# Optimization experiments

Hardware: AMD Instinct MI355X
Metric: run time of the kernel (lower is better)

Reference implementation:

```python
import jax, jax.numpy as jnp
import numpy as np

D = 256; NH = 8; NL = 4; NP = 4; DFF = 2048; HD = D // NH
SHAPES = [(64, 64), (32, 32), (16, 16), (8, 8)]
B = 2; LEN = sum(h * w for h, w in SHAPES)


def setup_inputs() -> dict:
    key = jax.random.key(0)
    ks = jax.random.split(key, 12)
    def w(k, shape, s=0.02):
        return jax.random.normal(k, shape, jnp.float32) * s
    starts = np.cumsum([0] + [h * w for h, w in SHAPES[:-1]])
    return {
        "src": jax.random.normal(ks[0], (B, LEN, D), jnp.float32),
        "pos": jax.random.normal(ks[1], (B, LEN, D), jnp.float32) * 0.1,
        "spatial_shapes": jnp.array(SHAPES, dtype=jnp.int32),
        "level_start_index": jnp.array(starts, dtype=jnp.int32),
        "w_value": w(ks[2], (D, D)), "b_value": jnp.zeros((D,), jnp.float32),
        "w_off": w(ks[3], (D, NH * NL * NP * 2)), "b_off": w(ks[4], (NH * NL * NP * 2,), 0.1),
        "w_attn": w(ks[5], (D, NH * NL * NP)), "b_attn": jnp.zeros((NH * NL * NP,), jnp.float32),
        "w_out": w(ks[6], (D, D)), "b_out": jnp.zeros((D,), jnp.float32),
        "w1": w(ks[7], (D, DFF)), "b1": jnp.zeros((DFF,), jnp.float32),
        "w2": w(ks[8], (DFF, D)), "b2": jnp.zeros((D,), jnp.float32),
        "g1": jnp.ones((D,), jnp.float32), "be1": jnp.zeros((D,), jnp.float32),
        "g2": jnp.ones((D,), jnp.float32), "be2": jnp.zeros((D,), jnp.float32),
    }


def _layer_norm(x, g, b):
    mu = jnp.mean(x, -1, keepdims=True)
    v = jnp.var(x, -1, keepdims=True)
    return (x - mu) * jax.lax.rsqrt(v + 1e-5) * g + b


def _reference_points(shapes):
    # torch.linspace(0.5, H-0.5, H)/H == (arange(H)+0.5)/H
    refs = []
    for H, W in shapes:
        ry = (jnp.arange(H, dtype=jnp.float32) + 0.5) / H
        rx = (jnp.arange(W, dtype=jnp.float32) + 0.5) / W
        yy, xx = jnp.meshgrid(ry, rx, indexing='ij')
        refs.append(jnp.stack([xx.ravel(), yy.ravel()], -1))
    return jnp.concatenate(refs, 0)  # (Len, 2) as (x, y)


def _ms_deform_sample(value, loc, shapes):
    # value: (B, Len, NH, HD); loc: (B, Lq, NH, NL, NP, 2) normalized [0,1]
    # Replicates torch grid_sample(bilinear, padding='zeros', align_corners=False).
    Bn, Lq = loc.shape[0], loc.shape[1]
    P = loc.shape[4]
    start = 0
    outs = []
    for lvl, (H, W) in enumerate(shapes):
        v = value[:, start:start + H * W].transpose(0, 2, 1, 3)  # (B, NH, HW, HD)
        start += H * W
        l = loc[:, :, :, lvl]                      # (B, Lq, NH, P, 2)
        x = l[..., 0] * W - 0.5
        y = l[..., 1] * H - 0.5
        x0 = jnp.floor(x); y0 = jnp.floor(y)
        dx = x - x0; dy = y - y0
        x0i = x0.astype(jnp.int32); y0i = y0.astype(jnp.int32)
        acc = None
        for xi, yi, wgt in ((x0i, y0i, (1 - dx) * (1 - dy)),
                            (x0i + 1, y0i, dx * (1 - dy)),
                            (x0i, y0i + 1, (1 - dx) * dy),
                            (x0i + 1, y0i + 1, dx * dy)):
            valid = ((xi >= 0) & (xi < W) & (yi >= 0) & (yi < H)).astype(value.dtype)
            idx = jnp.clip(yi, 0, H - 1) * W + jnp.clip(xi, 0, W - 1)  # (B, Lq, NH, P)
            idx = idx.transpose(0, 2, 1, 3).reshape(Bn, NH, Lq * P)
            g = jnp.take_along_axis(v, idx[..., None], axis=2).reshape(Bn, NH, Lq, P, HD)
            w = (wgt * valid).transpose(0, 2, 1, 3)[..., None]  # (B, NH, Lq, P, 1)
            acc = g * w if acc is None else acc + g * w
        outs.append(acc)  # (B, NH, Lq, P, HD)
    return jnp.stack(outs, 3)  # (B, NH, Lq, NL, NP, HD)


def _forward(src, pos, w_value, b_value, w_off, b_off, w_attn, b_attn,
             w_out, b_out, w1, b1, w2, b2, g1, be1, g2, be2, shapes):
    Bn, Lq, _ = src.shape
    q = src + pos  # with_pos_embed
    value = (src @ w_value + b_value).reshape(Bn, Lq, NH, HD)
    off = (q @ w_off + b_off).reshape(Bn, Lq, NH, NL, NP, 2)
    attn = jax.nn.softmax((q @ w_attn + b_attn).reshape(Bn, Lq, NH, NL * NP), -1)
    attn = attn.reshape(Bn, Lq, NH, NL, NP)
    ref = _reference_points(shapes)  # (Len, 2)
    normalizer = jnp.array([[w_, h_] for h_, w_ in shapes], jnp.float32)  # (NL, 2) = (W, H)
    loc = ref[None, :, None, None, None, :] + off / normalizer[None, None, None, :, None, :]
    sampled = _ms_deform_sample(value, loc, shapes)  # (B, NH, Lq, NL, NP, HD)
    out = jnp.einsum('bqhlp,bhqlpd->bqhd', attn, sampled).reshape(Bn, Lq, D)
    out = out @ w_out + b_out
    x = _layer_norm(src + out, g1, be1)           # residual + norm1
    ff = jax.nn.relu(x @ w1 + b1) @ w2 + b2       # FFN (dropout=0)
    return _layer_norm(x + ff, g2, be2)           # residual + norm2


def reference(src, pos, spatial_shapes, level_start_index, w_value, b_value,
              w_off, b_off, w_attn, b_attn, w_out, b_out, w1, b1, w2, b2,
              g1, be1, g2, be2):
    shapes = [tuple(int(v) for v in s) for s in np.asarray(spatial_shapes)]
    return _forward(src, pos, w_value, b_value, w_off, b_off, w_attn, b_attn,
                    w_out, b_out, w1, b1, w2, b2, g1, be1, g2, be2, shapes)
```

## Files before the change

### kernel.cpp

```cpp
#include <hip/hip_runtime.h>
#include <math.h>

#define D 256
#define NH 8
#define NL 4
#define NP 4
#define DFF 2048
#define HD 32
#define BB 2
#define LEN 5440
#define MROWS (BB * LEN)

typedef __attribute__((ext_vector_type(8))) short short8;
typedef __attribute__((ext_vector_type(4))) float f32x4;
typedef unsigned int uint32;

__device__ __forceinline__ unsigned short f2bf(float f) {
    uint32 u = __float_as_uint(f);
    u += 0x7FFF + ((u >> 16) & 1);
    return (unsigned short)(u >> 16);
}
__device__ __forceinline__ float bf2f(unsigned short h) {
    return __uint_as_float(((uint32)h) << 16);
}
__device__ __forceinline__ uint32 pack2(float a, float b) {
    return (uint32)f2bf(a) | ((uint32)f2bf(b) << 16);
}

__device__ __forceinline__ void swz85(int b, int ncols, int& row, int& col) {
    const int gsz = ncols << 3;
    const int full = 10 * gsz;
    if (b < full) {
        const int g = b / gsz, idx = b - g * gsz;
        row = (g << 3) + (idx & 7);
        col = idx >> 3;
    } else {
        const int idx = b - full;
        row = 80 + idx % 5;
        col = idx / 5;
    }
}

__global__ void prep(const float* __restrict__ w_value, const float* __restrict__ w_off,
                     const float* __restrict__ w_attn, const float* __restrict__ w_out,
                     const float* __restrict__ w1, const float* __restrict__ w2,
                     const float* __restrict__ b_value, const float* __restrict__ b_off,
                     const float* __restrict__ b_attn,
                     unsigned short* __restrict__ wqvT, unsigned short* __restrict__ woT,
                     unsigned short* __restrict__ w1T, unsigned short* __restrict__ w2T,
                     float* __restrict__ bqv) {
    const int blk = blockIdx.x;
    if (blk >= 1248) {
        for (int i = threadIdx.x; i < 640; i += 256)
            bqv[i] = (i < 256) ? b_value[i] : (i < 512 ? b_off[i - 256] : b_attn[i - 512]);
        return;
    }
    const float* W; unsigned short* WT; int K, N, tid;
    if (blk < 64)       { W = w_value; WT = wqvT;             K = 256;  N = 256;  tid = blk; }
    else if (blk < 128) { W = w_off;   WT = wqvT + 256 * 256; K = 256;  N = 256;  tid = blk - 64; }
    else if (blk < 160) { W = w_attn;  WT = wqvT + 512 * 256; K = 256;  N = 128;  tid = blk - 128; }
    else if (blk < 224) { W = w_out;   WT = woT;              K = 256;  N = 256;  tid = blk - 160; }
    else if (blk < 736) { W = w1;      WT = w1T;              K = 256;  N = 2048; tid = blk - 224; }
    else                { W = w2;      WT = w2T;              K = 2048; N = 256;  tid = blk - 736; }
    const int ntx = N >> 5;
    const int nb = (tid % ntx) * 32, kb = (tid / ntx) * 32;

    __shared__ float tile[32][33];
    const int tx = threadIdx.x & 31, ty = threadIdx.x >> 5;
#pragma unroll
    for (int i = 0; i < 32; i += 8)
        tile[ty + i][tx] = W[(size_t)(kb + ty + i) * N + nb + tx];
    __syncthreads();
#pragma unroll
    for (int i = 0; i < 32; i += 8)
        WT[(size_t)(nb + ty + i) * K + kb + tx] = f2bf(tile[tx][ty + i]);
}

__global__ __launch_bounds__(256) void ffn1_gemm(
        const unsigned short* __restrict__ A,
        const unsigned short* __restrict__ BT, const float* __restrict__ bias,
        unsigned short* __restrict__ Cv, int N, int K, int lda, int ldb) {
    __shared__ unsigned short Ash[128][40];
    __shared__ unsigned short Bsh[128][40];

    int rowt, colt;
    swz85(blockIdx.x, N >> 7, rowt, colt);
    const int row0 = rowt * 128, col0 = colt * 128;

    const int t = threadIdx.x;
    const int wave = t >> 6, lane = t & 63;
    const int wr = wave >> 1, wc = wave & 1;
    const int lrow = lane & 15, quad = lane >> 4;
    const int srow = t >> 1;
    const int cb = (t & 1) * 16;

    const unsigned short* ap = A + (size_t)(row0 + srow) * lda + cb;
    const unsigned short* bp = BT + (size_t)(col0 + srow) * ldb + cb;

    f32x4 acc[4][4];
#pragma unroll
    for (int i = 0; i < 4; i++)
#pragma unroll
        for (int j = 0; j < 4; j++) acc[i][j] = (f32x4){0.f, 0.f, 0.f, 0.f};

    uint4 ra0 = *(const uint4*)(ap + 0), ra1 = *(const uint4*)(ap + 8);
    uint4 rb0 = *(const uint4*)(bp + 0), rb1 = *(const uint4*)(bp + 8);

    for (int kb = 0; kb < K; kb += 32) {
        __syncthreads();
        *(uint4*)&Ash[srow][cb + 0] = ra0;
        *(uint4*)&Ash[srow][cb + 8] = ra1;
        *(uint4*)&Bsh[srow][cb + 0] = rb0;
        *(uint4*)&Bsh[srow][cb + 8] = rb1;
        __syncthreads();
        if (kb + 32 < K) {
            ra0 = *(const uint4*)(ap + kb + 32 + 0);
            ra1 = *(const uint4*)(ap + kb + 32 + 8);
            rb0 = *(const uint4*)(bp + kb + 32 + 0);
            rb1 = *(const uint4*)(bp + kb + 32 + 8);
        }

        short8 af[4], bfr[4];
#pragma unroll
        for (int mt = 0; mt < 4; mt++)
            af[mt] = *(const short8*)&Ash[wr * 64 + mt * 16 + lrow][quad * 8];
#pragma unroll
        for (int nt = 0; nt < 4; nt++)
            bfr[nt] = *(const short8*)&Bsh[wc * 64 + nt * 16 + lrow][quad * 8];
#pragma unroll
        for (int mt = 0; mt < 4; mt++)
#pragma unroll
            for (int nt = 0; nt < 4; nt++)
                acc[mt][nt] = __builtin_amdgcn_mfma_f32_16x16x32_bf16(
                    af[mt], bfr[nt], acc[mt][nt], 0, 0, 0);
    }

#pragma unroll
    for (int nt = 0; nt < 4; nt++) {
        const int col = col0 + wc * 64 + nt * 16 + lrow;
        const float bv = bias[col];
#pragma unroll
        for (int mt = 0; mt < 4; mt++) {
            f32x4 a = acc[mt][nt];
#pragma unroll
            for (int r = 0; r < 4; r++) {
                const int row = row0 + wr * 64 + mt * 16 + quad * 4 + r;
                Cv[(size_t)row * N + col] = f2bf(fmaxf(a[r] + bv, 0.f));
            }
        }
    }
}

template <int NZ>
__global__ __launch_bounds__(256) void splitk_gemm(
        const unsigned short* __restrict__ A, const unsigned short* __restrict__ BT,
        float* __restrict__ part, int KC, int lda, int ldb) {
    __shared__ unsigned short Ash[128][40];
    __shared__ unsigned short Bsh[128][40];

    int rowt, cc;
    swz85(blockIdx.x, 2 * NZ, rowt, cc);
    const int row0 = rowt * 128;
    const int col0 = (cc & 1) * 128;
    const int z = cc >> 1;
    const int koff = z * KC;
    float* __restrict__ C = part + (size_t)z * MROWS * 256;

    const int t = threadIdx.x;
    const int wave = t >> 6, lane = t & 63;
    const int wr = wave >> 1, wc = wave & 1;
    const int lrow = lane & 15, quad = lane >> 4;
    const int srow = t >> 1;
    const int cb = (t & 1) * 16;

    const unsigned short* ap = A + (size_t)(row0 + srow) * lda + koff + cb;
    const unsigned short* bp = BT + (size_t)(col0 + srow) * ldb + koff + cb;

    f32x4 acc[4][4];
#pragma unroll
    for (int i = 0; i < 4; i++)
#pragma unroll
        for (int j = 0; j < 4; j++) acc[i][j] = (f32x4){0.f, 0.f, 0.f, 0.f};

    uint4 ra0 = *(const uint4*)(ap + 0), ra1 = *(const uint4*)(ap + 8);
    uint4 rb0 = *(const uint4*)(bp + 0), rb1 = *(const uint4*)(bp + 8);

    for (int kb = 0; kb < KC; kb += 32) {
        __syncthreads();
        *(uint4*)&Ash[srow][cb + 0] = ra0;
        *(uint4*)&Ash[srow][cb + 8] = ra1;
        *(uint4*)&Bsh[srow][cb + 0] = rb0;
        *(uint4*)&Bsh[srow][cb + 8] = rb1;
        __syncthreads();
        if (kb + 32 < KC) {
            ra0 = *(const uint4*)(ap + kb + 32 + 0);
            ra1 = *(const uint4*)(ap + kb + 32 + 8);
            rb0 = *(const uint4*)(bp + kb + 32 + 0);
            rb1 = *(const uint4*)(bp + kb + 32 + 8);
        }

        short8 af[4], bfr[4];
#pragma unroll
        for (int mt = 0; mt < 4; mt++)
            af[mt] = *(const short8*)&Ash[wr * 64 + mt * 16 + lrow][quad * 8];
#pragma unroll
        for (int nt = 0; nt < 4; nt++)
            bfr[nt] = *(const short8*)&Bsh[wc * 64 + nt * 16 + lrow][quad * 8];
#pragma unroll
        for (int mt = 0; mt < 4; mt++)
#pragma unroll
            for (int nt = 0; nt < 4; nt++)
                acc[mt][nt] = __builtin_amdgcn_mfma_f32_16x16x32_bf16(
                    af[mt], bfr[nt], acc[mt][nt], 0, 0, 0);
    }

#pragma unroll
    for (int nt = 0; nt < 4; nt++) {
        const int col = col0 + wc * 64 + nt * 16 + lrow;
#pragma unroll
        for (int mt = 0; mt < 4; mt++) {
            f32x4 a = acc[mt][nt];
#pragma unroll
            for (int r = 0; r < 4; r++) {
                const int row = row0 + wr * 64 + mt * 16 + quad * 4 + r;
                C[(size_t)row * 256 + col] = a[r];
            }
        }
    }
}

__global__ __launch_bounds__(256) void qv_gemm(
        const float* __restrict__ src, const float* __restrict__ pos,
        const unsigned short* __restrict__ BT, const float* __restrict__ bias,
        unsigned short* __restrict__ val, float* __restrict__ qout) {
    __shared__ unsigned short Ash[128][40];
    __shared__ unsigned short Bsh[128][40];

    int rowt, colt;
    swz85(blockIdx.x, 5, rowt, colt);
    const int row0 = rowt * 128, col0 = colt * 128;
    const bool addp = (col0 >= 256);

    const int t = threadIdx.x;
    const int wave = t >> 6, lane = t & 63;
    const int wr = wave >> 1, wc = wave & 1;
    const int lrow = lane & 15, quad = lane >> 4;
    const int srow = t >> 1;
    const int cb = (t & 1) * 16;

    const float* ap = src + (size_t)(row0 + srow) * 256 + cb;
    const float* pp = pos + (size_t)(row0 + srow) * 256 + cb;
    const unsigned short* bp = BT + (size_t)(col0 + srow) * 256 + cb;

    f32x4 acc[4][4];
#pragma unroll
    for (int i = 0; i < 4; i++)
#pragma unroll
        for (int j = 0; j < 4; j++) acc[i][j] = (f32x4){0.f, 0.f, 0.f, 0.f};

    float4 fa[4]; float4 fp[4]; uint4 rb0, rb1;
#pragma unroll
    for (int j = 0; j < 4; j++) fa[j] = *(const float4*)(ap + 4 * j);
    if (addp) {
#pragma unroll
        for (int j = 0; j < 4; j++) fp[j] = *(const float4*)(pp + 4 * j);
    }
    rb0 = *(const uint4*)(bp + 0);
    rb1 = *(const uint4*)(bp + 8);

    for (int kb = 0; kb < 256; kb += 32) {
        __syncthreads();
        {
            float4 f0 = fa[0], f1 = fa[1], f2 = fa[2], f3 = fa[3];
            if (addp) {
                f0.x += fp[0].x; f0.y += fp[0].y; f0.z += fp[0].z; f0.w += fp[0].w;
                f1.x += fp[1].x; f1.y += fp[1].y; f1.z += fp[1].z; f1.w += fp[1].w;
                f2.x += fp[2].x; f2.y += fp[2].y; f2.z += fp[2].z; f2.w += fp[2].w;
                f3.x += fp[3].x; f3.y += fp[3].y; f3.z += fp[3].z; f3.w += fp[3].w;
            }
            uint4 u0 = make_uint4(pack2(f0.x, f0.y), pack2(f0.z, f0.w),
                                  pack2(f1.x, f1.y), pack2(f1.z, f1.w));
            uint4 u1 = make_uint4(pack2(f2.x, f2.y), pack2(f2.z, f2.w),
                                  pack2(f3.x, f3.y), pack2(f3.z, f3.w));
            *(uint4*)&Ash[srow][cb + 0] = u0;
            *(uint4*)&Ash[srow][cb + 8] = u1;
            *(uint4*)&Bsh[srow][cb + 0] = rb0;
            *(uint4*)&Bsh[srow][cb + 8] = rb1;
        }
        __syncthreads();
        if (kb + 32 < 256) {
#pragma unroll
            for (int j = 0; j < 4; j++) fa[j] = *(const float4*)(ap + kb + 32 + 4 * j);
            if (addp) {
#pragma unroll
                for (int j = 0; j < 4; j++) fp[j] = *(const float4*)(pp + kb + 32 + 4 * j);
            }
            rb0 = *(const uint4*)(bp + kb + 32 + 0);
            rb1 = *(const uint4*)(bp + kb + 32 + 8);
        }

        short8 af[4], bfr[4];
#pragma unroll
        for (int mt = 0; mt < 4; mt++)
            af[mt] = *(const short8*)&Ash[wr * 64 + mt * 16 + lrow][quad * 8];
#pragma unroll
        for (int nt = 0; nt < 4; nt++)
            bfr[nt] = *(const short8*)&Bsh[wc * 64 + nt * 16 + lrow][quad * 8];
#pragma unroll
        for (int mt = 0; mt < 4; mt++)
#pragma unroll
            for (int nt = 0; nt < 4; nt++)
                acc[mt][nt] = __builtin_amdgcn_mfma_f32_16x16x32_bf16(
                    af[mt], bfr[nt], acc[mt][nt], 0, 0, 0);
    }

#pragma unroll
    for (int nt = 0; nt < 4; nt++) {
        const int col = col0 + wc * 64 + nt * 16 + lrow;
        const float bv = bias[col];
#pragma unroll
        for (int mt = 0; mt < 4; mt++) {
            f32x4 a = acc[mt][nt];
#pragma unroll
            for (int r = 0; r < 4; r++) {
                const int row = row0 + wr * 64 + mt * 16 + quad * 4 + r;
                float v = a[r] + bv;
                if (col < 256)
                    val[(size_t)row * 256 + col] = f2bf(v);
                else
                    qout[(size_t)row * 384 + (col - 256)] = v;
            }
        }
    }
}

__global__ void sampler(const unsigned short* __restrict__ val, const float* __restrict__ qout,
                        unsigned short* __restrict__ out) {
    __shared__ __align__(16) int   sIdx[2][128][4];
    __shared__ __align__(16) float sW[2][128][4];
    const int t = threadIdx.x;
    const int sub = t >> 7;
    const int tt = t & 127;
    const int bq = blockIdx.x * 2 + sub;
    const int b = bq / LEN, q = bq % LEN;

    {
        const int h = tt >> 4, p = tt & 15;
        const int l = p >> 2;

        float refx, refy;
        if (q < 4096) {
            int rq = q >> 6, cq = q & 63;
            refx = (cq + 0.5f) * (1.0f / 64.0f);
            refy = (rq + 0.5f) * (1.0f / 64.0f);
        } else if (q < 5120) {
            int qq = q - 4096;
            int rq = qq >> 5, cq = qq & 31;
            refx = (cq + 0.5f) * (1.0f / 32.0f);
            refy = (rq + 0.5f) * (1.0f / 32.0f);
        } else if (q < 5376) {
            int qq = q - 5120;
            int rq = qq >> 4, cq = qq & 15;
            refx = (cq + 0.5f) * (1.0f / 16.0f);
            refy = (rq + 0.5f) * (1.0f / 16.0f);
        } else {
            int qq = q - 5376;
            int rq = qq >> 3, cq = qq & 7;
            refx = (cq + 0.5f) * (1.0f / 8.0f);
            refy = (rq + 0.5f) * (1.0f / 8.0f);
        }

        float lv = qout[(size_t)bq * 384 + 256 + tt];
        float mx = lv;
#pragma unroll
        for (int o = 1; o < 16; o <<= 1) mx = fmaxf(mx, __shfl_xor(mx, o, 16));
        float e = expf(lv - mx);
        float s = e;
#pragma unroll
        for (int o = 1; o < 16; o <<= 1) s += __shfl_xor(s, o, 16);
        const float aw = e / s;

        const float ox = qout[(size_t)bq * 384 + h * 32 + p * 2 + 0];
        const float oy = qout[(size_t)bq * 384 + h * 32 + p * 2 + 1];

        const int LST[4] = {0, 4096, 5120, 5376};
        const int WW = 64 >> l;
        const float rw = 1.0f / (float)WW;

        float x = (refx + ox * rw) * (float)WW - 0.5f;
        float y = (refy + oy * rw) * (float)WW - 0.5f;
        float x0f = floorf(x), y0f = floorf(y);
        float dx = x - x0f, dy = y - y0f;
        int x0 = (int)x0f, y0 = (int)y0f;

        const int base = (b * LEN + LST[l]) * 256 + h * 32;
        int xs[2] = {x0, x0 + 1}, ys[2] = {y0, y0 + 1};
        float wx[2] = {1.f - dx, dx}, wy[2] = {1.f - dy, dy};
        int ic[4]; float wc4[4];
#pragma unroll
        for (int cy = 0; cy < 2; cy++)
#pragma unroll
            for (int cx = 0; cx < 2; cx++) {
                int xi = xs[cx], yi = ys[cy];
                bool vld = (xi >= 0) && (xi < WW) && (yi >= 0) && (yi < WW);
                int xc = min(max(xi, 0), WW - 1);
                int yc = min(max(yi, 0), WW - 1);
                ic[cy * 2 + cx] = base + (yc * WW + xc) * 256;
                wc4[cy * 2 + cx] = vld ? wx[cx] * wy[cy] * aw : 0.f;
            }
        *(int4*)&sIdx[sub][tt][0] = make_int4(ic[0], ic[1], ic[2], ic[3]);
        *(float4*)&sW[sub][tt][0] = make_float4(wc4[0], wc4[1], wc4[2], wc4[3]);
    }
    __syncthreads();

    const int h = tt >> 4, dp = tt & 15;
    const unsigned short* vald = val + 2 * dp;
    float acc0 = 0.f, acc1 = 0.f;
#pragma unroll 4
    for (int p = 0; p < 16; p++) {
        const int r = h * 16 + p;
        int4 iv = *(const int4*)&sIdx[sub][r][0];
        float4 wv = *(const float4*)&sW[sub][r][0];
        uint32 u0 = *(const uint32*)(vald + iv.x);
        uint32 u1 = *(const uint32*)(vald + iv.y);
        uint32 u2 = *(const uint32*)(vald + iv.z);
        uint32 u3 = *(const uint32*)(vald + iv.w);
        acc0 += bf2f((unsigned short)u0) * wv.x + bf2f((unsigned short)u1) * wv.y +
                bf2f((unsigned short)u2) * wv.z + bf2f((unsigned short)u3) * wv.w;
        acc1 += bf2f((unsigned short)(u0 >> 16)) * wv.x + bf2f((unsigned short)(u1 >> 16)) * wv.y +
                bf2f((unsigned short)(u2 >> 16)) * wv.z + bf2f((unsigned short)(u3 >> 16)) * wv.w;
    }
    *(uint32*)&out[(size_t)bq * D + h * HD + 2 * dp] = pack2(acc0, acc1);
}

template <int NPART>
__global__ void add_lnN(const float* __restrict__ part, const float* __restrict__ bias,
                        const float* __restrict__ rsd,
                        const float* __restrict__ g, const float* __restrict__ be,
                        float* __restrict__ out, unsigned short* __restrict__ out16) {
    __shared__ float r1[4], r2[4];
    const int row = blockIdx.x, t = threadIdx.x;
    const size_t i = (size_t)row * D + t;
    float v = bias[t] + rsd[i];
#pragma unroll
    for (int z = 0; z < NPART; z++) v += part[(size_t)z * MROWS * 256 + i];
    float s1 = v, s2 = v * v;
#pragma unroll
    for (int o = 32; o > 0; o >>= 1) {
        s1 += __shfl_down(s1, o, 64);
        s2 += __shfl_down(s2, o, 64);
    }
    if ((t & 63) == 0) { r1[t >> 6] = s1; r2[t >> 6] = s2; }
    __syncthreads();
    float su = r1[0] + r1[1] + r1[2] + r1[3];
    float sq = r2[0] + r2[1] + r2[2] + r2[3];
    float mean = su * (1.0f / D);
    float var = fmaxf(sq * (1.0f / D) - mean * mean, 0.f);
    const float o = (v - mean) * rsqrtf(var + 1e-5f) * g[t] + be[t];
    out[i] = o;
    if (out16) out16[i] = f2bf(o);
}

extern "C" void kernel_launch(void* const* d_in, const int* in_sizes, int n_in,
                              void* d_out, int out_size, void* d_ws, size_t ws_size,
                              hipStream_t stream) {
    const float* src     = (const float*)d_in[0];
    const float* pos     = (const float*)d_in[1];
    const float* w_value = (const float*)d_in[4];
    const float* b_value = (const float*)d_in[5];
    const float* w_off   = (const float*)d_in[6];
    const float* b_off   = (const float*)d_in[7];
    const float* w_attn  = (const float*)d_in[8];
    const float* b_attn  = (const float*)d_in[9];
    const float* w_out   = (const float*)d_in[10];
    const float* b_out   = (const float*)d_in[11];
    const float* w1      = (const float*)d_in[12];
    const float* b1      = (const float*)d_in[13];
    const float* w2      = (const float*)d_in[14];
    const float* b2      = (const float*)d_in[15];
    const float* g1      = (const float*)d_in[16];
    const float* be1     = (const float*)d_in[17];
    const float* g2      = (const float*)d_in[18];
    const float* be2     = (const float*)d_in[19];
    float* out = (float*)d_out;

    size_t off = 0;
    auto alloc = [&](size_t bytes) -> char* {
        char* p = (char*)d_ws + off;
        off += (bytes + 255) & ~(size_t)255;
        return p;
    };
    unsigned short* wqvT = (unsigned short*)alloc((size_t)640 * 256 * 2);
    unsigned short* woT  = (unsigned short*)alloc(256 * 256 * 2);
    unsigned short* w1T  = (unsigned short*)alloc((size_t)2048 * 256 * 2);
    unsigned short* w2T  = (unsigned short*)alloc((size_t)256 * 2048 * 2);
    float* bqv           = (float*)alloc(640 * 4);

    float* qout          = (float*)alloc((size_t)MROWS * 384 * 4);
    unsigned short* val  = (unsigned short*)alloc((size_t)MROWS * 256 * 2);
    unsigned short* attn = (unsigned short*)alloc((size_t)MROWS * 256 * 2);
    unsigned short* hb   = (unsigned short*)alloc((size_t)MROWS * 2048 * 2);
    float* xbuf          = (float*)alloc((size_t)MROWS * 256 * 4);
    unsigned short* xb16 = (unsigned short*)alloc((size_t)MROWS * 256 * 2);
    float* part          = (float*)alloc((size_t)4 * MROWS * 256 * 4);

    prep<<<1249, 256, 0, stream>>>(w_value, w_off, w_attn, w_out, w1, w2,
                                   b_value, b_off, b_attn, wqvT, woT, w1T, w2T, bqv);

    qv_gemm<<<425, 256, 0, stream>>>(src, pos, wqvT, bqv, val, qout);
    sampler<<<MROWS / 2, 256, 0, stream>>>(val, qout, attn);
    splitk_gemm<2><<<340, 256, 0, stream>>>(attn, woT, part, 128, 256, 256);
    add_lnN<2><<<MROWS, 256, 0, stream>>>(part, b_out, src, g1, be1, xbuf, xb16);

    ffn1_gemm<<<1360, 256, 0, stream>>>(xb16, w1T, b1, hb, 2048, 256, 256, 256);
    splitk_gemm<4><<<680, 256, 0, stream>>>(hb, w2T, part, 512, 2048, 2048);
    add_lnN<4><<<MROWS, 256, 0, stream>>>(part, b2, xbuf, g2, be2, out, nullptr);
}
```

Measured before the change: 218.6 us.

## Fuse output GEMMs with bias, residual and LayerNorm in full-row tiles

Replaces the split-K GEMMs plus separate add+LayerNorm kernels with one kernel per stage. Each block computes 32 full rows of 256 columns and does bias, residual, mean/variance reduction and normalization in the epilogue. This removes the fp32 partial-sum buffers and their round trips through memory, and drops two launches. In exchange there is no split-K parallelism: only 340 blocks run, each looping over the full K (2048 for FFN2), and the tiles are small, so MFMA efficiency and occupancy may suffer.

```diff
diff --git a/kernel.cpp b/kernel.cpp
--- a/kernel.cpp
+++ b/kernel.cpp
@@ -151,82 +151,129 @@
     }
 }
 
-template <int NZ>
-__global__ __launch_bounds__(256) void splitk_gemm(
+template <bool WRITE16>
+__global__ __launch_bounds__(256) void gemm_ln(
         const unsigned short* __restrict__ A, const unsigned short* __restrict__ BT,
-        float* __restrict__ part, int KC, int lda, int ldb) {
-    __shared__ unsigned short Ash[128][40];
-    __shared__ unsigned short Bsh[128][40];
-
-    int rowt, cc;
-    swz85(blockIdx.x, 2 * NZ, rowt, cc);
-    const int row0 = rowt * 128;
-    const int col0 = (cc & 1) * 128;
-    const int z = cc >> 1;
-    const int koff = z * KC;
-    float* __restrict__ C = part + (size_t)z * MROWS * 256;
-
+        const float* __restrict__ bias, const float* __restrict__ rsd,
+        const float* __restrict__ g, const float* __restrict__ be,
+        float* __restrict__ out, unsigned short* __restrict__ out16, int K) {
+    __shared__ __align__(16) unsigned short Ash[32][40];
+    __shared__ __align__(16) unsigned short Bsh[256][40];
+    __shared__ float red1[4][32], red2[4][32];
+
+    const int row0 = blockIdx.x * 32;
     const int t = threadIdx.x;
     const int wave = t >> 6, lane = t & 63;
-    const int wr = wave >> 1, wc = wave & 1;
     const int lrow = lane & 15, quad = lane >> 4;
-    const int srow = t >> 1;
-    const int cb = (t & 1) * 16;
-
-    const unsigned short* ap = A + (size_t)(row0 + srow) * lda + koff + cb;
-    const unsigned short* bp = BT + (size_t)(col0 + srow) * ldb + koff + cb;
-
-    f32x4 acc[4][4];
-#pragma unroll
-    for (int i = 0; i < 4; i++)
+
+    const int ar = t >> 3, ac = (t & 7) * 4;
+    const unsigned short* ap = A + (size_t)(row0 + ar) * K + ac;
+    const int br = t >> 1, cb = (t & 1) * 16;
+    const unsigned short* bp0 = BT + (size_t)br * K + cb;
+    const unsigned short* bp1 = BT + (size_t)(128 + br) * K + cb;
+
+    f32x4 acc[2][4];
+#pragma unroll
+    for (int i = 0; i < 2; i++)
 #pragma unroll
         for (int j = 0; j < 4; j++) acc[i][j] = (f32x4){0.f, 0.f, 0.f, 0.f};
 
-    uint4 ra0 = *(const uint4*)(ap + 0), ra1 = *(const uint4*)(ap + 8);
-    uint4 rb0 = *(const uint4*)(bp + 0), rb1 = *(const uint4*)(bp + 8);
-
-    for (int kb = 0; kb < KC; kb += 32) {
+    uint2 ra = *(const uint2*)ap;
+    uint4 rb00 = *(const uint4*)(bp0 + 0), rb01 = *(const uint4*)(bp0 + 8);
+    uint4 rb10 = *(const uint4*)(bp1 + 0), rb11 = *(const uint4*)(bp1 + 8);
+
+    for (int kb = 0; kb < K; kb += 32) {
         __syncthreads();
-        *(uint4*)&Ash[srow][cb + 0] = ra0;
-        *(uint4*)&Ash[srow][cb + 8] = ra1;
-        *(uint4*)&Bsh[srow][cb + 0] = rb0;
-        *(uint4*)&Bsh[srow][cb + 8] = rb1;
+        *(uint2*)&Ash[ar][ac] = ra;
+        *(uint4*)&Bsh[br][cb + 0] = rb00;
+        *(uint4*)&Bsh[br][cb + 8] = rb01;
+        *(uint4*)&Bsh[128 + br][cb + 0] = rb10;
+        *(uint4*)&Bsh[128 + br][cb + 8] = rb11;
         __syncthreads();
-        if (kb + 32 < KC) {
-            ra0 = *(const uint4*)(ap + kb + 32 + 0);
-            ra1 = *(const uint4*)(ap + kb + 32 + 8);
-            rb0 = *(const uint4*)(bp + kb + 32 + 0);
-            rb1 = *(const uint4*)(bp + kb + 32 + 8);
-        }
-
-        short8 af[4], bfr[4];
-#pragma unroll
-        for (int mt = 0; mt < 4; mt++)
-            af[mt] = *(const short8*)&Ash[wr * 64 + mt * 16 + lrow][quad * 8];
+        if (kb + 32 < K) {
+            ra   = *(const uint2*)(ap + kb + 32);
+            rb00 = *(const uint4*)(bp0 + kb + 32 + 0);
+            rb01 = *(const uint4*)(bp0 + kb + 32 + 8);
+            rb10 = *(const uint4*)(bp1 + kb + 32 + 0);
+            rb11 = *(const uint4*)(bp1 + kb + 32 + 8);
+        }
+
+        short8 af[2], bfr[4];
+#pragma unroll
+        for (int mt = 0; mt < 2; mt++)
+            af[mt] = *(const short8*)&Ash[mt * 16 + lrow][quad * 8];
 #pragma unroll
         for (int nt = 0; nt < 4; nt++)
-            bfr[nt] = *(const short8*)&Bsh[wc * 64 + nt * 16 + lrow][quad * 8];
-#pragma unroll
-        for (int mt = 0; mt < 4; mt++)
+            bfr[nt] = *(const short8*)&Bsh[wave * 64 + nt * 16 + lrow][quad * 8];
+#pragma unroll
+        for (int mt = 0; mt < 2; mt++)
 #pragma unroll
             for (int nt = 0; nt < 4; nt++)
                 acc[mt][nt] = __builtin_amdgcn_mfma_f32_16x16x32_bf16(
                     af[mt], bfr[nt], acc[mt][nt], 0, 0, 0);
     }
 
+    float gv[4], bev[4], bv[4];
 #pragma unroll
     for (int nt = 0; nt < 4; nt++) {
-        const int col = col0 + wc * 64 + nt * 16 + lrow;
-#pragma unroll
-        for (int mt = 0; mt < 4; mt++) {
-            f32x4 a = acc[mt][nt];
-#pragma unroll
-            for (int r = 0; r < 4; r++) {
-                const int row = row0 + wr * 64 + mt * 16 + quad * 4 + r;
-                C[(size_t)row * 256 + col] = a[r];
-            }
-        }
-    }
+        const int col = wave * 64 + nt * 16 + lrow;
+        bv[nt] = bias[col];
+        gv[nt] = g[col];
+        bev[nt] = be[col];
+    }
+
+    float v[2][4][4];
+#pragma unroll
+    for (int mt = 0; mt < 2; mt++)
+#pragma unroll
+        for (int r = 0; r < 4; r++) {
+            const int row = row0 + mt * 16 + quad * 4 + r;
+#pragma unroll
+            for (int nt = 0; nt < 4; nt++) {
+                const int col = wave * 64 + nt * 16 + lrow;
+                v[mt][nt][r] = acc[mt][nt][r] + bv[nt] + rsd[(size_t)row * 256 + col];
+            }
+        }
+
+#pragma unroll
+    for (int mt = 0; mt < 2; mt++)
+#pragma unroll
+        for (int r = 0; r < 4; r++) {
+            float s1 = v[mt][0][r] + v[mt][1][r] + v[mt][2][r] + v[mt][3][r];
+            float s2 = v[mt][0][r] * v[mt][0][r] + v[mt][1][r] * v[mt][1][r] +
+                       v[mt][2][r] * v[mt][2][r] + v[mt][3][r] * v[mt][3][r];
+#pragma unroll
+            for (int o = 1; o < 16; o <<= 1) {
+                s1 += __shfl_xor(s1, o, 16);
+                s2 += __shfl_xor(s2, o, 16);
+            }
+            if (lrow == 0) {
+                const int rr = mt * 16 + quad * 4 + r;
+                red1[wave][rr] = s1;
+                red2[wave][rr] = s2;
+            }
+        }
+    __syncthreads();
+
+#pragma unroll
+    for (int mt = 0; mt < 2; mt++)
+#pragma unroll
+        for (int r = 0; r < 4; r++) {
+            const int rr = mt * 16 + quad * 4 + r;
+            const float su = red1[0][rr] + red1[1][rr] + red1[2][rr] + red1[3][rr];
+            const float sq = red2[0][rr] + red2[1][rr] + red2[2][rr] + red2[3][rr];
+            const float mean = su * (1.0f / 256.0f);
+            const float var = fmaxf(sq * (1.0f / 256.0f) - mean * mean, 0.f);
+            const float rstd = rsqrtf(var + 1e-5f);
+            const size_t rowoff = (size_t)(row0 + rr) * 256;
+#pragma unroll
+            for (int nt = 0; nt < 4; nt++) {
+                const int col = wave * 64 + nt * 16 + lrow;
+                const float o = (v[mt][nt][r] - mean) * rstd * gv[nt] + bev[nt];
+                out[rowoff + col] = o;
+                if (WRITE16) out16[rowoff + col] = f2bf(o);
+            }
+        }
 }
 
 __global__ __launch_bounds__(256) void qv_gemm(
@@ -431,34 +478,6 @@
                 bf2f((unsigned short)(u2 >> 16)) * wv.z + bf2f((unsigned short)(u3 >> 16)) * wv.w;
     }
     *(uint32*)&out[(size_t)bq * D + h * HD + 2 * dp] = pack2(acc0, acc1);
-}
-
-template <int NPART>
-__global__ void add_lnN(const float* __restrict__ part, const float* __restrict__ bias,
-                        const float* __restrict__ rsd,
-                        const float* __restrict__ g, const float* __restrict__ be,
-                        float* __restrict__ out, unsigned short* __restrict__ out16) {
-    __shared__ float r1[4], r2[4];
-    const int row = blockIdx.x, t = threadIdx.x;
-    const size_t i = (size_t)row * D + t;
-    float v = bias[t] + rsd[i];
-#pragma unroll
-    for (int z = 0; z < NPART; z++) v += part[(size_t)z * MROWS * 256 + i];
-    float s1 = v, s2 = v * v;
-#pragma unroll
-    for (int o = 32; o > 0; o >>= 1) {
-        s1 += __shfl_down(s1, o, 64);
-        s2 += __shfl_down(s2, o, 64);
-    }
-    if ((t & 63) == 0) { r1[t >> 6] = s1; r2[t >> 6] = s2; }
-    __syncthreads();
-    float su = r1[0] + r1[1] + r1[2] + r1[3];
-    float sq = r2[0] + r2[1] + r2[2] + r2[3];
-    float mean = su * (1.0f / D);
-    float var = fmaxf(sq * (1.0f / D) - mean * mean, 0.f);
-    const float o = (v - mean) * rsqrtf(var + 1e-5f) * g[t] + be[t];
-    out[i] = o;
-    if (out16) out16[i] = f2bf(o);
 }
 
 extern "C" void kernel_launch(void* const* d_in, const int* in_sizes, int n_in,
@@ -502,17 +521,16 @@
     unsigned short* hb   = (unsigned short*)alloc((size_t)MROWS * 2048 * 2);
     float* xbuf          = (float*)alloc((size_t)MROWS * 256 * 4);
     unsigned short* xb16 = (unsigned short*)alloc((size_t)MROWS * 256 * 2);
-    float* part          = (float*)alloc((size_t)4 * MROWS * 256 * 4);
 
     prep<<<1249, 256, 0, stream>>>(w_value, w_off, w_attn, w_out, w1, w2,
                                    b_value, b_off, b_attn, wqvT, woT, w1T, w2T, bqv);
 
     qv_gemm<<<425, 256, 0, stream>>>(src, pos, wqvT, bqv, val, qout);
     sampler<<<MROWS / 2, 256, 0, stream>>>(val, qout, attn);
-    splitk_gemm<2><<<340, 256, 0, stream>>>(attn, woT, part, 128, 256, 256);
-    add_lnN<2><<<MROWS, 256, 0, stream>>>(part, b_out, src, g1, be1, xbuf, xb16);
+    gemm_ln<true><<<340, 256, 0, stream>>>(attn, woT, b_out, src, g1, be1,
+                                           xbuf, xb16, 256);
 
     ffn1_gemm<<<1360, 256, 0, stream>>>(xb16, w1T, b1, hb, 2048, 256, 256, 256);
-    splitk_gemm<4><<<680, 256, 0, stream>>>(hb, w2T, part, 512, 2048, 2048);
-    add_lnN<4><<<MROWS, 256, 0, stream>>>(part, b2, xbuf, g2, be2, out, nullptr);
-}
+    gemm_ln<false><<<340, 256, 0, stream>>>(hb, w2T, b2, xbuf, g2, be2,
+                                            out, nullptr, 2048);
+}
```

New measurement: 224.5 us. 1.03x slower.
